# Optimization experiments

Hardware: AMD Instinct MI355X
Metric: run time of the kernel (lower is better)

## Reference

```python
import jax, jax.numpy as jnp
import numpy as np
import math

B, S, E, H = 4, 2048, 1024, 16
HD = E // H

def setup_inputs() -> dict:
    key = jax.random.key(0)
    ks = jax.random.split(key, 5)
    lim_qkv = math.sqrt(6.0 / (E + 3 * E))  # xavier_uniform for (3E, E)
    lim_out = math.sqrt(6.0 / (E + E))
    return {
        "x": jax.random.normal(ks[0], (B, S, E), dtype=jnp.float32),
        "qkv_w": jax.random.uniform(ks[1], (3 * E, E), minval=-lim_qkv, maxval=lim_qkv, dtype=jnp.float32),
        "qkv_b": jnp.zeros((3 * E,), dtype=jnp.float32),
        "out_w": jax.random.uniform(ks[2], (E, E), minval=-lim_out, maxval=lim_out, dtype=jnp.float32),
        "out_b": jnp.zeros((E,), dtype=jnp.float32),
    }

def reference(x, qkv_w, qkv_b, out_w, out_b):
    bsz, seq_len, embed_dim = x.shape
    scale = math.sqrt(HD)
    # fused QKV projection (torch Linear: x @ W.T + b)
    qkv = x @ qkv_w.T + qkv_b                      # [B, S, 3E]
    # per-head layout: slice [h*3hd:(h+1)*3hd] holds (q,k,v) for head h
    qkv = qkv.reshape(bsz, seq_len, H, 3, HD)       # [B, S, H, 3, hd]
    q = jnp.transpose(qkv[:, :, :, 0, :], (0, 2, 1, 3))  # [B, H, S, hd]
    k = jnp.transpose(qkv[:, :, :, 1, :], (0, 2, 1, 3))
    v = jnp.transpose(qkv[:, :, :, 2, :], (0, 2, 1, 3))
    scores = jnp.einsum("bhqd,bhkd->bhqk", q, k) / scale
    causal = jnp.tril(jnp.ones((seq_len, seq_len), dtype=bool))
    scores = jnp.where(causal[None, None], scores, -jnp.inf)
    attn = jax.nn.softmax(scores, axis=-1)          # dropout = identity (eval mode)
    out = jnp.einsum("bhqk,bhkd->bhqd", attn, v)    # [B, H, S, hd]
    out = jnp.transpose(out, (0, 2, 1, 3)).reshape(bsz, seq_len, embed_dim)
    return out @ out_w.T + out_b
```

## Files before the change

### kernel.cpp

```cpp
#include <hip/hip_runtime.h>
#include <hip/hip_bf16.h>
#include <cstdint>

#define NB 4
#define NS 2048
#define NE 1024
#define NH 16

typedef __attribute__((ext_vector_type(8))) short bf16x8;
typedef __attribute__((ext_vector_type(4))) float f32x4;

__device__ __forceinline__ unsigned short f2bf(float f) {
  unsigned u = __float_as_uint(f);
  u += 0x7fffu + ((u >> 16) & 1u);
  return (unsigned short)(u >> 16);
}

__device__ __forceinline__ unsigned cvtpk(float lo, float hi) {
  unsigned r;
  asm("v_cvt_pk_bf16_f32 %0, %1, %2" : "=v"(r) : "v"(lo), "v"(hi));
  return r;
}

__device__ __forceinline__ float exp2_fast(float x) {
#if __has_builtin(__builtin_amdgcn_exp2f)
  return __builtin_amdgcn_exp2f(x);
#else
  float r;
  asm("v_exp_f32 %0, %1" : "=v"(r) : "v"(x));
  return r;
#endif
}

__device__ __forceinline__ void gl_lds16(const void* g, void* l) {
  __builtin_amdgcn_global_load_lds(
      (const __attribute__((address_space(1))) void*)g,
      (__attribute__((address_space(3))) void*)l, 16, 0, 0);
}

__global__ __launch_bounds__(256) void cast3_k(const float* __restrict__ x,
                                               const float* __restrict__ w1,
                                               const float* __restrict__ w2,
                                               unsigned short* __restrict__ out) {
  int idx = blockIdx.x * 256 + threadIdx.x;
  const float4* src;
  int local = idx;
  if (idx < 2097152) {
    src = (const float4*)x;
  } else if (idx < 2883584) {
    src = (const float4*)w1; local = idx - 2097152;
  } else {
    src = (const float4*)w2; local = idx - 2883584;
  }
  float4 v = src[local];
  ushort4 o;
  o.x = f2bf(v.x); o.y = f2bf(v.y); o.z = f2bf(v.z); o.w = f2bf(v.w);
  ((ushort4*)out)[idx] = o;
}

template <int MODE>
__global__ __launch_bounds__(256, 2) void gemm_bt(
    const unsigned short* __restrict__ A,
    const unsigned short* __restrict__ Bm,
    const float* __restrict__ bias,
    void* __restrict__ Cv,
    unsigned short* __restrict__ Qp,
    unsigned short* __restrict__ Kp,
    unsigned short* __restrict__ Vp,
    int M, int N, int K) {
  __shared__ __align__(16) unsigned short As[128 * 64];
  __shared__ __align__(16) unsigned short Bs[128 * 64];
  const int tid = threadIdx.x;
  const int lane = tid & 63, wave = tid >> 6;
  const int m0 = blockIdx.y * 128, n0 = blockIdx.x * 128;
  const int wm = (wave >> 1) * 64, wn = (wave & 1) * 64;
  const int fr = lane & 15, fq = lane >> 4;

  f32x4 acc[4][4];
#pragma unroll
  for (int i = 0; i < 4; i++)
#pragma unroll
    for (int j = 0; j < 4; j++) acc[i][j] = (f32x4){0.f, 0.f, 0.f, 0.f};

  const int srow = lane >> 3;
  const int scol = ((lane & 7) ^ srow) * 8;

  for (int kt = 0; kt < K; kt += 64) {
    __syncthreads();
#pragma unroll
    for (int c = 0; c < 4; c++) {
      const int chunk = wave * 4 + c;
      const int row = chunk * 8 + srow;
      gl_lds16(A + (size_t)(m0 + row) * K + kt + scol, As + chunk * 512);
      gl_lds16(Bm + (size_t)(n0 + row) * K + kt + scol, Bs + chunk * 512);
    }
    __syncthreads();
#pragma unroll
    for (int s = 0; s < 2; s++) {
      bf16x8 af[4], bf[4];
#pragma unroll
      for (int i = 0; i < 4; i++)
        af[i] = *(const bf16x8*)(As + (wm + i * 16 + fr) * 64 +
                                 (((s * 4 + fq) ^ (fr & 7)) * 8));
#pragma unroll
      for (int j = 0; j < 4; j++)
        bf[j] = *(const bf16x8*)(Bs + (wn + j * 16 + fr) * 64 +
                                 (((s * 4 + fq) ^ (fr & 7)) * 8));
#pragma unroll
      for (int i = 0; i < 4; i++)
#pragma unroll
        for (int j = 0; j < 4; j++)
          acc[i][j] = __builtin_amdgcn_mfma_f32_16x16x32_bf16(af[i], bf[j], acc[i][j], 0, 0, 0);
    }
  }

#pragma unroll
  for (int j = 0; j < 4; j++) {
    const int col = n0 + wn + j * 16 + fr;
    const float bval = bias[col];
    if (MODE == 0) {
#pragma unroll
      for (int i = 0; i < 4; i++)
#pragma unroll
        for (int r = 0; r < 4; r++) {
          const int row = m0 + wm + i * 16 + fq * 4 + r;
          ((float*)Cv)[(size_t)row * N + col] = acc[i][j][r] + bval;
        }
    } else {
      const int h = col / 192, rr = col - h * 192;
      if (rr < 64) {
#pragma unroll
        for (int i = 0; i < 4; i++)
#pragma unroll
          for (int r = 0; r < 4; r++) {
            const int row = m0 + wm + i * 16 + fq * 4 + r;
            const int b = row >> 11, s = row & 2047;
            Qp[((size_t)(b * 16 + h) * 2048 + s) * 64 + rr] =
                f2bf((acc[i][j][r] + bval) * 0.1803368802f);
          }
      } else if (rr < 128) {
#pragma unroll
        for (int i = 0; i < 4; i++)
#pragma unroll
          for (int r = 0; r < 4; r++) {
            const int row = m0 + wm + i * 16 + fq * 4 + r;
            const int b = row >> 11, s = row & 2047;
            Kp[((size_t)(b * 16 + h) * 2048 + s) * 64 + (rr - 64)] =
                f2bf(acc[i][j][r] + bval);
          }
      } else {
#pragma unroll
        for (int i = 0; i < 4; i++) {
          const int row0 = m0 + wm + i * 16 + fq * 4;
          const int b = row0 >> 11, s = row0 & 2047;
          ushort4 o;
          o.x = f2bf(acc[i][j][0] + bval);
          o.y = f2bf(acc[i][j][1] + bval);
          o.z = f2bf(acc[i][j][2] + bval);
          o.w = f2bf(acc[i][j][3] + bval);
          *(ushort4*)(Vp + ((size_t)(b * 16 + h) * 64 + (rr - 128)) * 2048 + s) = o;
        }
      }
    }
  }
}

__global__ __launch_bounds__(128, 2) void attn_k(
    const unsigned short* __restrict__ Qg, const unsigned short* __restrict__ Kg,
    const unsigned short* __restrict__ Vg, unsigned short* __restrict__ outa) {
  __shared__ __align__(16) unsigned short Ks[2 * 64 * 64];
  __shared__ __align__(16) unsigned short VTs[2 * 64 * 64];
  __shared__ __align__(16) unsigned short Ps[2 * 32 * 64];
  const int tid = threadIdx.x;
  const int lane = tid & 63, wave = tid >> 6;
  const int fc = lane & 15, fq = lane >> 4, fc7 = fc & 7;
  const int wg = ((int)blockIdx.x & 7) * 128 + ((int)blockIdx.x >> 3);
  const int bh = wg >> 4, qx = wg & 15;
  const int b = bh >> 4, h = bh & 15;
  const int srow = lane >> 3;
  const int scol = ((lane & 7) ^ srow) * 8;
  const int pswz = fc & 14;
  const unsigned short* Qb = Qg + (size_t)bh * 2048 * 64;
  const unsigned short* Kb = Kg + (size_t)bh * 2048 * 64;
  const unsigned short* Vb = Vg + (size_t)bh * 64 * 2048;
  unsigned short* Pw = Ps + wave * 32 * 64;
  bf16x8 vones;
#pragma unroll
  for (int j = 0; j < 8; j++) vones[j] = (short)0x3F80;

#pragma unroll 1
  for (int phase = 0; phase < 2; phase++) {
    const int qt = phase ? 31 - qx : qx;
    const int qw = qt * 64 + wave * 32;

    bf16x8 qb[2][2];
#pragma unroll
    for (int g = 0; g < 2; g++) {
      const unsigned short* qrow = Qb + (size_t)(qw + g * 16 + fc) * 64;
      qb[g][0] = *(const bf16x8*)(qrow + fq * 8);
      qb[g][1] = *(const bf16x8*)(qrow + 32 + fq * 8);
    }

    f32x4 O[4][2];
#pragma unroll
    for (int dt = 0; dt < 4; dt++)
#pragma unroll
      for (int g = 0; g < 2; g++) O[dt][g] = (f32x4){0.f, 0.f, 0.f, 0.f};
    f32x4 O1[2];
#pragma unroll
    for (int g = 0; g < 2; g++) O1[g] = (f32x4){0.f, 0.f, 0.f, 0.f};
    f32x4 cz[2];
#pragma unroll
    for (int g = 0; g < 2; g++) cz[g] = (f32x4){0.f, 0.f, 0.f, 0.f};

#pragma unroll
    for (int c = 0; c < 4; c++) {
      const int rbase = c * 16 + wave * 8;
      gl_lds16(Kb + (size_t)(rbase + srow) * 64 + scol, Ks + rbase * 64);
      gl_lds16(Vb + (size_t)(rbase + srow) * 2048 + scol, VTs + rbase * 64);
    }
    __syncthreads();

#pragma unroll 1
    for (int kb = 0; kb <= qt; kb++) {
      const int bsel = kb & 1;
      if (kb < qt) {
        const size_t koff = (size_t)(kb + 1) * 4096;
        const int voff = (kb + 1) * 64;
        unsigned short* Kd = Ks + (bsel ^ 1) * 4096;
        unsigned short* Vd = VTs + (bsel ^ 1) * 4096;
#pragma unroll
        for (int c = 0; c < 4; c++) {
          const int rbase = c * 16 + wave * 8;
          gl_lds16(Kb + koff + (size_t)(rbase + srow) * 64 + scol, Kd + rbase * 64);
          gl_lds16(Vb + (size_t)(rbase + srow) * 2048 + voff + scol, Vd + rbase * 64);
        }
      }
      const int k0 = kb * 64;
      const unsigned short* Ksb = Ks + bsel * 4096;
      const unsigned short* VTb = VTs + bsel * 4096;

      f32x4 S[4][2];
      __builtin_amdgcn_s_setprio(1);
#pragma unroll
      for (int t = 0; t < 4; t++) {
        bf16x8 ka0 = *(const bf16x8*)(Ksb + (t * 16 + fc) * 64 + ((fq ^ fc7) * 8));
        bf16x8 ka1 = *(const bf16x8*)(Ksb + (t * 16 + fc) * 64 + (((4 + fq) ^ fc7) * 8));
#pragma unroll
        for (int g = 0; g < 2; g++) {
          f32x4 s = __builtin_amdgcn_mfma_f32_16x16x32_bf16(ka0, qb[g][0], cz[g], 0, 0, 0);
          S[t][g] = __builtin_amdgcn_mfma_f32_16x16x32_bf16(ka1, qb[g][1], s, 0, 0, 0);
        }
      }
      __builtin_amdgcn_s_setprio(0);
      if (kb == qt) {
#pragma unroll
        for (int t = 0; t < 4; t++)
#pragma unroll
          for (int g = 0; g < 2; g++)
#pragma unroll
            for (int r = 0; r < 4; r++)
              if (k0 + t * 16 + fq * 4 + r > qw + g * 16 + fc) S[t][g][r] = -3e38f;
      }
      float alpha[2] = {1.f, 1.f};
      bool resc = false;
#pragma unroll
      for (int g = 0; g < 2; g++) {
        float a0 = fmaxf(fmaxf(S[0][g][0], S[0][g][1]), S[0][g][2]);
        float a1 = fmaxf(fmaxf(S[0][g][3], S[1][g][0]), S[1][g][1]);
        float a2 = fmaxf(fmaxf(S[1][g][2], S[1][g][3]), S[2][g][0]);
        float a3 = fmaxf(fmaxf(S[2][g][1], S[2][g][2]), S[2][g][3]);
        float a4 = fmaxf(fmaxf(S[3][g][0], S[3][g][1]), S[3][g][2]);
        float b0 = fmaxf(fmaxf(a0, a1), a2);
        float b1 = fmaxf(fmaxf(a3, a4), S[3][g][3]);
        float cm = fmaxf(b0, b1);
        if (!__all(cm <= 8.0f)) {
          cm = fmaxf(cm, __shfl_xor(cm, 16, 64));
          cm = fmaxf(cm, __shfl_xor(cm, 32, 64));
          const float delta = fmaxf(cm, 0.f);
          alpha[g] = exp2_fast(-delta);
#pragma unroll
          for (int r = 0; r < 4; r++) cz[g][r] -= delta;
#pragma unroll
          for (int t = 0; t < 4; t++)
#pragma unroll
            for (int r = 0; r < 4; r++) S[t][g][r] -= delta;
          resc = true;
        }
#pragma unroll
        for (int t = 0; t < 4; t++)
#pragma unroll
          for (int r = 0; r < 4; r++) S[t][g][r] = exp2_fast(S[t][g][r]);
      }
#pragma unroll
      for (int g = 0; g < 2; g++)
#pragma unroll
        for (int t = 0; t < 4; t++) {
          uint2 u;
          u.x = cvtpk(S[t][g][0], S[t][g][1]);
          u.y = cvtpk(S[t][g][2], S[t][g][3]);
          *(uint2*)(Pw + (g * 16 + fc) * 64 + (((t * 4 + fq) ^ pswz) * 4)) = u;
        }
      bf16x8 pb[2][2];
#pragma unroll
      for (int g = 0; g < 2; g++)
#pragma unroll
        for (int s = 0; s < 2; s++)
          pb[g][s] = *(const bf16x8*)(Pw + (g * 16 + fc) * 64 +
                                      (((s * 8 + fq * 2) ^ pswz) * 4));
      if (resc) {
#pragma unroll
        for (int dt = 0; dt < 4; dt++)
#pragma unroll
          for (int g = 0; g < 2; g++)
#pragma unroll
            for (int r = 0; r < 4; r++) O[dt][g][r] *= alpha[g];
#pragma unroll
        for (int g = 0; g < 2; g++)
#pragma unroll
          for (int r = 0; r < 4; r++) O1[g][r] *= alpha[g];
      }
      __builtin_amdgcn_s_setprio(1);
#pragma unroll
      for (int dt = 0; dt < 4; dt++) {
        bf16x8 va0 = *(const bf16x8*)(VTb + (dt * 16 + fc) * 64 + ((fq ^ fc7) * 8));
        bf16x8 va1 = *(const bf16x8*)(VTb + (dt * 16 + fc) * 64 + (((4 + fq) ^ fc7) * 8));
#pragma unroll
        for (int g = 0; g < 2; g++) {
          O[dt][g] = __builtin_amdgcn_mfma_f32_16x16x32_bf16(va0, pb[g][0], O[dt][g], 0, 0, 0);
          O[dt][g] = __builtin_amdgcn_mfma_f32_16x16x32_bf16(va1, pb[g][1], O[dt][g], 0, 0, 0);
        }
      }
#pragma unroll
      for (int g = 0; g < 2; g++) {
        O1[g] = __builtin_amdgcn_mfma_f32_16x16x32_bf16(vones, pb[g][0], O1[g], 0, 0, 0);
        O1[g] = __builtin_amdgcn_mfma_f32_16x16x32_bf16(vones, pb[g][1], O1[g], 0, 0, 0);
      }
      __builtin_amdgcn_s_setprio(0);
      __syncthreads();
    }

    float inv[2];
#pragma unroll
    for (int g = 0; g < 2; g++) inv[g] = 1.f / O1[g][0];
#pragma unroll
    for (int dt = 0; dt < 4; dt++)
#pragma unroll
      for (int g = 0; g < 2; g++) {
        uint2 u;
        u.x = cvtpk(O[dt][g][0] * inv[g], O[dt][g][1] * inv[g]);
        u.y = cvtpk(O[dt][g][2] * inv[g], O[dt][g][3] * inv[g]);
        size_t row = (size_t)(b * NS) + qw + g * 16 + fc;
        *(uint2*)(outa + row * 1024 + h * 64 + dt * 16 + fq * 4) = u;
      }
  }
}

extern "C" void kernel_launch(void* const* d_in, const int* in_sizes, int n_in,
                              void* d_out, int out_size, void* d_ws, size_t ws_size,
                              hipStream_t stream) {
  const float* x     = (const float*)d_in[0];
  const float* qkv_w = (const float*)d_in[1];
  const float* qkv_b = (const float*)d_in[2];
  const float* out_w = (const float*)d_in[3];
  const float* out_b = (const float*)d_in[4];

  unsigned short* xb   = (unsigned short*)d_ws;
  unsigned short* wqkv = xb + (size_t)8192 * 1024;
  unsigned short* wo   = wqkv + (size_t)3072 * 1024;
  unsigned short* Qg   = wo + (size_t)1024 * 1024;
  unsigned short* Kg   = Qg + (size_t)64 * 2048 * 64;
  unsigned short* Vg   = Kg + (size_t)64 * 2048 * 64;
  unsigned short* att  = Vg + (size_t)64 * 64 * 2048;

  cast3_k<<<12288, 256, 0, stream>>>(x, qkv_w, out_w, xb);

  gemm_bt<1><<<dim3(24, 64), 256, 0, stream>>>(xb, wqkv, qkv_b, nullptr,
                                               Qg, Kg, Vg, 8192, 3072, 1024);
  attn_k<<<dim3(1024), 128, 0, stream>>>(Qg, Kg, Vg, att);
  gemm_bt<0><<<dim3(8, 64), 256, 0, stream>>>(att, wo, out_b, d_out,
                                              nullptr, nullptr, nullptr,
                                              8192, 1024, 1024);
}
```

Measured before the change: 245.1 us.

## Double-buffer LDS tiles in GEMM to overlap global loads with MFMA

The projection GEMM kernel now keeps two LDS buffers for the A and B tiles. It issues the next k-tile's global-to-LDS loads before computing on the current tile, and uses one barrier per iteration instead of two, so global-load latency is hidden behind MFMA work. This doubles shared memory to 64KB per block, which can limit how many blocks fit per CU alongside launch_bounds(256,2). Address computation is also hoisted out of the loop.

```diff
diff --git a/kernel.cpp b/kernel.cpp
--- a/kernel.cpp
+++ b/kernel.cpp
@@ -68,8 +68,8 @@
     unsigned short* __restrict__ Kp,
     unsigned short* __restrict__ Vp,
     int M, int N, int K) {
-  __shared__ __align__(16) unsigned short As[128 * 64];
-  __shared__ __align__(16) unsigned short Bs[128 * 64];
+  __shared__ __align__(16) unsigned short As[2 * 128 * 64];
+  __shared__ __align__(16) unsigned short Bs[2 * 128 * 64];
   const int tid = threadIdx.x;
   const int lane = tid & 63, wave = tid >> 6;
   const int m0 = blockIdx.y * 128, n0 = blockIdx.x * 128;
@@ -84,27 +84,41 @@
 
   const int srow = lane >> 3;
   const int scol = ((lane & 7) ^ srow) * 8;
-
-  for (int kt = 0; kt < K; kt += 64) {
-    __syncthreads();
-#pragma unroll
-    for (int c = 0; c < 4; c++) {
-      const int chunk = wave * 4 + c;
-      const int row = chunk * 8 + srow;
-      gl_lds16(A + (size_t)(m0 + row) * K + kt + scol, As + chunk * 512);
-      gl_lds16(Bm + (size_t)(n0 + row) * K + kt + scol, Bs + chunk * 512);
-    }
-    __syncthreads();
+  const unsigned short* Ast = A + (size_t)(m0 + wave * 32 + srow) * K + scol;
+  const unsigned short* Bst = Bm + (size_t)(n0 + wave * 32 + srow) * K + scol;
+
+  const int nk = K >> 6;
+#pragma unroll
+  for (int c = 0; c < 4; c++) {
+    gl_lds16(Ast + (size_t)c * 8 * K, As + (wave * 4 + c) * 512);
+    gl_lds16(Bst + (size_t)c * 8 * K, Bs + (wave * 4 + c) * 512);
+  }
+  __syncthreads();
+
+  for (int ki = 0; ki < nk; ki++) {
+    const int bsel = ki & 1;
+    if (ki + 1 < nk) {
+      const int kt = (ki + 1) << 6;
+      unsigned short* Ad = As + (bsel ^ 1) * 8192;
+      unsigned short* Bd = Bs + (bsel ^ 1) * 8192;
+#pragma unroll
+      for (int c = 0; c < 4; c++) {
+        gl_lds16(Ast + (size_t)c * 8 * K + kt, Ad + (wave * 4 + c) * 512);
+        gl_lds16(Bst + (size_t)c * 8 * K + kt, Bd + (wave * 4 + c) * 512);
+      }
+    }
+    const unsigned short* Asb = As + bsel * 8192;
+    const unsigned short* Bsb = Bs + bsel * 8192;
 #pragma unroll
     for (int s = 0; s < 2; s++) {
       bf16x8 af[4], bf[4];
 #pragma unroll
       for (int i = 0; i < 4; i++)
-        af[i] = *(const bf16x8*)(As + (wm + i * 16 + fr) * 64 +
+        af[i] = *(const bf16x8*)(Asb + (wm + i * 16 + fr) * 64 +
                                  (((s * 4 + fq) ^ (fr & 7)) * 8));
 #pragma unroll
       for (int j = 0; j < 4; j++)
-        bf[j] = *(const bf16x8*)(Bs + (wn + j * 16 + fr) * 64 +
+        bf[j] = *(const bf16x8*)(Bsb + (wn + j * 16 + fr) * 64 +
                                  (((s * 4 + fq) ^ (fr & 7)) * 8));
 #pragma unroll
       for (int i = 0; i < 4; i++)
@@ -112,6 +126,7 @@
         for (int j = 0; j < 4; j++)
           acc[i][j] = __builtin_amdgcn_mfma_f32_16x16x32_bf16(af[i], bf[j], acc[i][j], 0, 0, 0);
     }
+    __syncthreads();
   }
 
 #pragma unroll
```

New measurement: 243.7 us. Within noise of the previous version (-0.6%).
